# Optimization experiments

Measured on AMD Instinct MI355X. Metric: run time of the kernel, lower is better.

The kernel has to match this reference:

```python
import jax, jax.numpy as jnp
import numpy as np

NUM_M = 512
NUM_T = 64
MAX_STEPS = 20
TAU = 1.0


def setup_inputs() -> dict:
    key = jax.random.key(0)
    ks = jax.random.split(key, 10)
    num_m, num_t = NUM_M, NUM_T
    inp = {
        "v_src": jax.random.normal(ks[0], (1, num_m), jnp.float32),
        "v_target": jax.random.normal(ks[1], (1, num_m), jnp.float32),
        # small-magnitude generators so matrix_exp stays well-conditioned
        "omegas": jax.random.normal(ks[2], (num_t, num_m, num_m), jnp.float32) * 0.01,
        "W1": jax.random.normal(ks[3], (2 * num_m, 256), jnp.float32) * (1.0 / np.sqrt(2 * num_m)),
        "b1": jnp.zeros((256,), jnp.float32),
        "W2": jax.random.normal(ks[4], (256, 128), jnp.float32) * (1.0 / np.sqrt(256)),
        "b2": jnp.zeros((128,), jnp.float32),
        "W3": jax.random.normal(ks[5], (128, num_t), jnp.float32) * (1.0 / np.sqrt(128)),
        "b3": jnp.zeros((num_t,), jnp.float32),
        # pre-sampled gumbel noise, one draw per step: [max_steps, B, num_t]
        "gumbel_noise": jax.random.gumbel(ks[6], (MAX_STEPS, 1, num_t), jnp.float32),
    }
    return inp


def reference(v_src, v_target, omegas, W1, b1, W2, b2, W3, b3, gumbel_noise):
    tgt_idx = jnp.argmax(v_target, axis=-1)  # [B]

    def mlp(x):
        h = jax.nn.relu(x @ W1 + b1)
        h = jax.nn.relu(h @ W2 + b2)
        return h @ W3 + b3  # [B, num_t]

    batched_expm = jax.vmap(jax.scipy.linalg.expm)

    def step(carry, g):
        v, done = carry  # v: [B, num_m], done: [B] bool
        x = jnp.concatenate([v, v_target], axis=-1)        # [B, 2*num_m]
        logits = mlp(x)                                     # [B, num_t]
        # gumbel_softmax(tau=1.0, hard=False)
        soft = jax.nn.softmax((logits + g) / TAU, axis=-1)
        omega_k = jnp.einsum('bt,tmk->bmk', soft, omegas)   # [B, m, m]
        R_k = batched_expm(omega_k)                         # [B, m, m]
        v_new = jnp.einsum('bmk,bk->bm', R_k, v)            # [B, m]
        # freeze state and zero-pad logits once the target marking was reached
        v_out = jnp.where(done[:, None], v, v_new)
        logits_out = jnp.where(done[:, None], jnp.zeros_like(logits), logits)
        done_new = done | (jnp.argmax(v_new, axis=-1) == tgt_idx)
        return (v_out, done_new), logits_out

    done0 = jnp.zeros((v_src.shape[0],), bool)
    (v_final, _), logits_seq = jax.lax.scan(step, (v_src, done0), gumbel_noise)
    # logits_seq: [max_steps, B, num_t]; B==1 -> [max_steps, num_t] (torch squeeze(0))
    return v_final, logits_seq[:, 0, :]
```

## Files before the change

### kernel.cpp

```cpp
#include <hip/hip_runtime.h>
#include <hip/hip_fp16.h>


#define NBLK 256
#define NTHR 512
#define NSTEP 20
#define NTAY 3
#define RBUF 4

typedef unsigned long long ull;

#define XW(buf, i) (X + ((((buf) << 8) + (i)) << 3))

__device__ __forceinline__ float wredsum(float p) {
#pragma unroll
  for (int off = 32; off > 0; off >>= 1) p += __shfl_xor(p, off, 64);
  return p;
}

__device__ __forceinline__ void publish2(ull* w, float v0, float v1, unsigned int tag2) {
  unsigned int u0 = (__float_as_uint(v0) & ~3u) | tag2;
  ull x = (ull)u0 | ((ull)__float_as_uint(v1) << 32);
  __hip_atomic_store(w, x, __ATOMIC_RELAXED, __HIP_MEMORY_SCOPE_AGENT);
}

__device__ __forceinline__ float2 poll2(ull* w, unsigned int tag2) {
  int it = 0;
  for (;;) {
    ull x = __hip_atomic_load(w, __ATOMIC_RELAXED, __HIP_MEMORY_SCOPE_AGENT);
    if ((unsigned int)(x & 3u) == tag2) {
      float2 r;
      r.x = __uint_as_float((unsigned int)x);
      r.y = __uint_as_float((unsigned int)(x >> 32));
      return r;
    }
    if (it == 0)      __builtin_amdgcn_s_sleep(1);
    else if (it == 1) __builtin_amdgcn_s_sleep(2);
    else              __builtin_amdgcn_s_sleep(4);
    if (it < 2) ++it;
  }
}

__global__ __launch_bounds__(NTHR) void petri_kernel(
    const float* __restrict__ vsrc, const float* __restrict__ vtgt,
    const float* __restrict__ omg,  const float* __restrict__ W1,
    const float* __restrict__ b1,   const float* __restrict__ W2,
    const float* __restrict__ b2,   const float* __restrict__ W3,
    const float* __restrict__ b3,   const float* __restrict__ gum,
    ull* __restrict__ X, float* __restrict__ out) {
  __shared__ __half2 oh[64 * 512];
  __shared__ float A0_s[512], A1_s[512];
  __shared__ float v_loc[512], tgt_s[512], w_s[512];
  __shared__ float w1c_s[1024];
  __shared__ float gum_s[NSTEP * 64];
  __shared__ float b2_s[128], b3_s[64];
  __shared__ float soft_s[64], h1_s[256], h2_s[128];
  __shared__ float redp[512];
  __shared__ float rf8[8];
  __shared__ int   ri8[8];
  __shared__ float acc2[2];
  __shared__ int   bc[1];

  const int b = blockIdx.x, tid = threadIdx.x;
  const int wv = tid >> 6, ln = tid & 63;

  v_loc[tid] = vsrc[tid];
  tgt_s[tid] = vtgt[tid];
  w1c_s[tid] = W1[tid * 256 + b];
  w1c_s[tid + 512] = W1[(tid + 512) * 256 + b];
  for (int i = tid; i < NSTEP * 64; i += NTHR) gum_s[i] = gum[i];
  if (tid >= 512 - 128) {
    int j = tid - (512 - 128);
    b2_s[j] = b2[j];
    if (j < 64) b3_s[j] = b3[j];
  }
  float w2r[64];
  {
    const int o = tid & 127, q = tid >> 7;
    const float* p = W2 + ((q << 6) * 128) + o;
#pragma unroll
    for (int i = 0; i < 64; ++i) w2r[i] = p[i * 128];
  }
  float w3r[16];
  {
    const int o = tid & 63, q = tid >> 6;
    const float* p = W3 + ((q << 4) * 64) + o;
#pragma unroll
    for (int i = 0; i < 16; ++i) w3r[i] = p[i * 64];
  }
  {
    const float* base0 = omg + (b << 10) + tid;
#pragma unroll 4
    for (int t = 0; t < 64; ++t) {
      float x0 = base0[t * 262144];
      float x1 = base0[t * 262144 + 512];
      oh[t * 512 + tid] = __floats2half2_rn(x0, x1);
    }
  }
  __syncthreads();

  int tgtIdx;
  {
    float v = tgt_s[tid]; int ix = tid;
#pragma unroll
    for (int off = 32; off > 0; off >>= 1) {
      float ov = __shfl_xor(v, off, 64); int oi = __shfl_xor(ix, off, 64);
      if (ov > v || (ov == v && oi < ix)) { v = ov; ix = oi; }
    }
    if (ln == 0) { rf8[wv] = v; ri8[wv] = ix; }
    __syncthreads();
    if (tid == 0) {
      float bv = rf8[0]; int bix = ri8[0];
      for (int q = 1; q < 8; ++q)
        if (rf8[q] > bv || (rf8[q] == bv && ri8[q] < bix)) { bv = rf8[q]; bix = ri8[q]; }
      bc[0] = bix;
    }
    __syncthreads();
    tgtIdx = bc[0];
    __syncthreads();
  }

  int d = 0;
  int r = 0;

  for (int s = 0; s < NSTEP; ++s) {
    if (d) {
      if (b == 0 && tid < 64) out[512 + s * 64 + tid] = 0.0f;
      continue;
    }

    {
      const int buf = r & (RBUF - 1);
      const unsigned int tg = (unsigned int)((r >> 2) & 3);
      float p = fmaf(v_loc[tid], w1c_s[tid], tgt_s[tid] * w1c_s[tid + 512]);
      p = wredsum(p);
      if (ln == 0) rf8[wv] = p;
      __syncthreads();
      if (tid == 0) {
        float a = b1[b];
        for (int q = 0; q < 8; ++q) a += rf8[q];
        float h = fmaxf(a, 0.f);
        publish2(XW(buf, b), h, h, tg);
      }
      if (tid < 256) h1_s[tid] = poll2(XW(buf, tid), tg).x;
      __syncthreads();
      ++r;
    }

    {
      const int q = tid >> 7;
      float a = 0.f;
      const float* hp = h1_s + (q << 6);
#pragma unroll
      for (int i = 0; i < 64; ++i) a = fmaf(hp[i], w2r[i], a);
      redp[tid] = a;
    }
    __syncthreads();
    if (tid < 128) {
      float rr = redp[tid] + redp[tid + 128] + redp[tid + 256] + redp[tid + 384] + b2_s[tid];
      h2_s[tid] = fmaxf(rr, 0.f);
    }
    __syncthreads();
    {
      const int q = tid >> 6;
      float a = 0.f;
      const float* hp = h2_s + (q << 4);
#pragma unroll
      for (int i = 0; i < 16; ++i) a = fmaf(hp[i], w3r[i], a);
      redp[tid] = a;
    }
    __syncthreads();
    if (tid < 64) {
      float a = b3_s[tid];
#pragma unroll
      for (int q = 0; q < 8; ++q) a += redp[tid + (q << 6)];
      float lg = a + gum_s[s * 64 + tid];
      float mx = lg;
#pragma unroll
      for (int off = 32; off > 0; off >>= 1) mx = fmaxf(mx, __shfl_xor(mx, off, 64));
      float e = __expf(lg - mx);
      float sm = e;
#pragma unroll
      for (int off = 32; off > 0; off >>= 1) sm += __shfl_xor(sm, off, 64);
      soft_s[tid] = e / sm;
      if (b == 0) out[512 + s * 64 + tid] = a;
    }
    __syncthreads();

    {
      float a0 = 0.f, a1 = 0.f;
#pragma unroll 8
      for (int t = 0; t < 64; ++t) {
        float2 xy = __half22float2(oh[t * 512 + tid]);
        float sv = soft_s[t];
        a0 = fmaf(sv, xy.x, a0);
        a1 = fmaf(sv, xy.y, a1);
      }
      A0_s[tid] = a0; A1_s[tid] = a1;
    }
    __syncthreads();

    {
      const int buf = r & (RBUF - 1);
      const unsigned int tg = (unsigned int)((r >> 2) & 3);
      const float* Ar = (tid < 256) ? A0_s : A1_s;
      const int j = tid & 255;
      float p = fmaf(Ar[j], v_loc[j], Ar[j + 256] * v_loc[j + 256]);
      p = wredsum(p);
      if (ln == 0) rf8[wv] = p;
      __syncthreads();
      if (tid == 0) {
        float s0 = rf8[0] + rf8[1] + rf8[2] + rf8[3];
        float s1 = rf8[4] + rf8[5] + rf8[6] + rf8[7];
        acc2[0] = v_loc[(b << 1)] + s0;
        acc2[1] = v_loc[(b << 1) + 1] + s1;
        publish2(XW(buf, b), s0, s1, tg);
      }
      if (tid < 256) {
        float2 g = poll2(XW(buf, tid), tg);
        w_s[(tid << 1)] = g.x;
        w_s[(tid << 1) + 1] = g.y;
      }
      __syncthreads();
      ++r;
    }

    for (int n = 2; n <= NTAY; ++n) {
      const int buf = r & (RBUF - 1);
      const unsigned int tg = (unsigned int)((r >> 2) & 3);
      const float* Ar = (tid < 256) ? A0_s : A1_s;
      const int j = tid & 255;
      float p = fmaf(Ar[j], w_s[j], Ar[j + 256] * w_s[j + 256]);
      p = wredsum(p);
      if (ln == 0) rf8[wv] = p;
      __syncthreads();
      if (tid == 0) {
        const float inv = 1.0f / (float)n;
        float s0 = (rf8[0] + rf8[1] + rf8[2] + rf8[3]) * inv;
        float s1 = (rf8[4] + rf8[5] + rf8[6] + rf8[7]) * inv;
        acc2[0] += s0; acc2[1] += s1;
        float p0 = (n < NTAY) ? s0 : acc2[0];
        float p1 = (n < NTAY) ? s1 : acc2[1];
        publish2(XW(buf, b), p0, p1, tg);
      }
      if (n < NTAY) {
        if (tid < 256) {
          float2 g = poll2(XW(buf, tid), tg);
          w_s[(tid << 1)] = g.x;
          w_s[(tid << 1) + 1] = g.y;
        }
        __syncthreads();
        ++r;
      } else {
        if (tid < 256) {
          float2 g = poll2(XW(buf, tid), tg);
          v_loc[(tid << 1)] = g.x;
          v_loc[(tid << 1) + 1] = g.y;
        }
        __syncthreads();
        float v = v_loc[tid]; int ix = tid;
#pragma unroll
        for (int off = 32; off > 0; off >>= 1) {
          float ov = __shfl_xor(v, off, 64); int oi = __shfl_xor(ix, off, 64);
          if (ov > v || (ov == v && oi < ix)) { v = ov; ix = oi; }
        }
        if (ln == 0) { rf8[wv] = v; ri8[wv] = ix; }
        __syncthreads();
        if (tid == 0) {
          float bv = rf8[0]; int bix = ri8[0];
          for (int q = 1; q < 8; ++q)
            if (rf8[q] > bv || (rf8[q] == bv && ri8[q] < bix)) { bv = rf8[q]; bix = ri8[q]; }
          bc[0] = (bix == tgtIdx) ? 1 : 0;
        }
        __syncthreads();
        if (bc[0]) d = 1;
        __syncthreads();
        ++r;
      }
    }
  }

  if (b == 0) out[tid] = v_loc[tid];
}

extern "C" void kernel_launch(void* const* d_in, const int* in_sizes, int n_in,
                              void* d_out, int out_size, void* d_ws, size_t ws_size,
                              hipStream_t stream) {
  (void)in_sizes; (void)n_in; (void)out_size; (void)ws_size;
  petri_kernel<<<dim3(NBLK), dim3(NTHR), 0, stream>>>(
      (const float*)d_in[0], (const float*)d_in[1], (const float*)d_in[2],
      (const float*)d_in[3], (const float*)d_in[4], (const float*)d_in[5],
      (const float*)d_in[6], (const float*)d_in[7], (const float*)d_in[8],
      (const float*)d_in[9], (ull*)d_ws, (float*)d_out);
}
```

Measured before the change: 364.0 us.

## Replicate cross-block exchange slots to spread polling contention

Each block now publishes its value to up to 8 replicated slots, and each group of blocks polls its own replica, so fewer pollers hit the same cache lines. The backoff sleeps in the poll loop are removed so waiting blocks spin tightly. The ring shrinks from 4 to 2 buffers, which shortens the tag cycle, and the replica count is chosen to fit the workspace. The cost is more stores per publish and heavier memory traffic from tight spinning.

```diff
diff --git a/kernel.cpp b/kernel.cpp
--- a/kernel.cpp
+++ b/kernel.cpp
@@ -6,11 +6,9 @@
 #define NTHR 512
 #define NSTEP 20
 #define NTAY 3
-#define RBUF 4
+#define RBUF 2
 
 typedef unsigned long long ull;
-
-#define XW(buf, i) (X + ((((buf) << 8) + (i)) << 3))
 
 __device__ __forceinline__ float wredsum(float p) {
 #pragma unroll
@@ -18,14 +16,21 @@
   return p;
 }
 
-__device__ __forceinline__ void publish2(ull* w, float v0, float v1, unsigned int tag2) {
+__device__ __forceinline__ ull* xw(ull* X, int buf, int word, int rep, int k) {
+  return X + ((((buf << 8) + word) << k) + rep) * 8;
+}
+
+__device__ __forceinline__ void publishR(ull* X, int buf, int word, int k,
+                                         float v0, float v1, unsigned int tag2) {
   unsigned int u0 = (__float_as_uint(v0) & ~3u) | tag2;
   ull x = (ull)u0 | ((ull)__float_as_uint(v1) << 32);
-  __hip_atomic_store(w, x, __ATOMIC_RELAXED, __HIP_MEMORY_SCOPE_AGENT);
-}
-
-__device__ __forceinline__ float2 poll2(ull* w, unsigned int tag2) {
-  int it = 0;
+  const int nrep = 1 << k;
+  for (int rp = 0; rp < nrep; ++rp)
+    __hip_atomic_store(xw(X, buf, word, rp, k), x, __ATOMIC_RELAXED,
+                       __HIP_MEMORY_SCOPE_AGENT);
+}
+
+__device__ __forceinline__ float2 pollR(ull* w, unsigned int tag2) {
   for (;;) {
     ull x = __hip_atomic_load(w, __ATOMIC_RELAXED, __HIP_MEMORY_SCOPE_AGENT);
     if ((unsigned int)(x & 3u) == tag2) {
@@ -34,10 +39,6 @@
       r.y = __uint_as_float((unsigned int)(x >> 32));
       return r;
     }
-    if (it == 0)      __builtin_amdgcn_s_sleep(1);
-    else if (it == 1) __builtin_amdgcn_s_sleep(2);
-    else              __builtin_amdgcn_s_sleep(4);
-    if (it < 2) ++it;
   }
 }
 
@@ -47,7 +48,7 @@
     const float* __restrict__ b1,   const float* __restrict__ W2,
     const float* __restrict__ b2,   const float* __restrict__ W3,
     const float* __restrict__ b3,   const float* __restrict__ gum,
-    ull* __restrict__ X, float* __restrict__ out) {
+    ull* __restrict__ X, float* __restrict__ out, int repk) {
   __shared__ __half2 oh[64 * 512];
   __shared__ float A0_s[512], A1_s[512];
   __shared__ float v_loc[512], tgt_s[512], w_s[512];
@@ -63,6 +64,7 @@
 
   const int b = blockIdx.x, tid = threadIdx.x;
   const int wv = tid >> 6, ln = tid & 63;
+  const int myrep = (b << repk) >> 8;
 
   v_loc[tid] = vsrc[tid];
   tgt_s[tid] = vtgt[tid];
@@ -131,7 +133,7 @@
 
     {
       const int buf = r & (RBUF - 1);
-      const unsigned int tg = (unsigned int)((r >> 2) & 3);
+      const unsigned int tg = (unsigned int)((r >> 1) & 3);
       float p = fmaf(v_loc[tid], w1c_s[tid], tgt_s[tid] * w1c_s[tid + 512]);
       p = wredsum(p);
       if (ln == 0) rf8[wv] = p;
@@ -140,9 +142,9 @@
         float a = b1[b];
         for (int q = 0; q < 8; ++q) a += rf8[q];
         float h = fmaxf(a, 0.f);
-        publish2(XW(buf, b), h, h, tg);
-      }
-      if (tid < 256) h1_s[tid] = poll2(XW(buf, tid), tg).x;
+        publishR(X, buf, b, repk, h, h, tg);
+      }
+      if (tid < 256) h1_s[tid] = pollR(xw(X, buf, tid, myrep, repk), tg).x;
       __syncthreads();
       ++r;
     }
@@ -202,7 +204,7 @@
 
     {
       const int buf = r & (RBUF - 1);
-      const unsigned int tg = (unsigned int)((r >> 2) & 3);
+      const unsigned int tg = (unsigned int)((r >> 1) & 3);
       const float* Ar = (tid < 256) ? A0_s : A1_s;
       const int j = tid & 255;
       float p = fmaf(Ar[j], v_loc[j], Ar[j + 256] * v_loc[j + 256]);
@@ -214,10 +216,10 @@
         float s1 = rf8[4] + rf8[5] + rf8[6] + rf8[7];
         acc2[0] = v_loc[(b << 1)] + s0;
         acc2[1] = v_loc[(b << 1) + 1] + s1;
-        publish2(XW(buf, b), s0, s1, tg);
+        publishR(X, buf, b, repk, s0, s1, tg);
       }
       if (tid < 256) {
-        float2 g = poll2(XW(buf, tid), tg);
+        float2 g = pollR(xw(X, buf, tid, myrep, repk), tg);
         w_s[(tid << 1)] = g.x;
         w_s[(tid << 1) + 1] = g.y;
       }
@@ -227,7 +229,7 @@
 
     for (int n = 2; n <= NTAY; ++n) {
       const int buf = r & (RBUF - 1);
-      const unsigned int tg = (unsigned int)((r >> 2) & 3);
+      const unsigned int tg = (unsigned int)((r >> 1) & 3);
       const float* Ar = (tid < 256) ? A0_s : A1_s;
       const int j = tid & 255;
       float p = fmaf(Ar[j], w_s[j], Ar[j + 256] * w_s[j + 256]);
@@ -241,11 +243,11 @@
         acc2[0] += s0; acc2[1] += s1;
         float p0 = (n < NTAY) ? s0 : acc2[0];
         float p1 = (n < NTAY) ? s1 : acc2[1];
-        publish2(XW(buf, b), p0, p1, tg);
+        publishR(X, buf, b, repk, p0, p1, tg);
       }
       if (n < NTAY) {
         if (tid < 256) {
-          float2 g = poll2(XW(buf, tid), tg);
+          float2 g = pollR(xw(X, buf, tid, myrep, repk), tg);
           w_s[(tid << 1)] = g.x;
           w_s[(tid << 1) + 1] = g.y;
         }
@@ -253,7 +255,7 @@
         ++r;
       } else {
         if (tid < 256) {
-          float2 g = poll2(XW(buf, tid), tg);
+          float2 g = pollR(xw(X, buf, tid, myrep, repk), tg);
           v_loc[(tid << 1)] = g.x;
           v_loc[(tid << 1) + 1] = g.y;
         }
@@ -286,10 +288,13 @@
 extern "C" void kernel_launch(void* const* d_in, const int* in_sizes, int n_in,
                               void* d_out, int out_size, void* d_ws, size_t ws_size,
                               hipStream_t stream) {
-  (void)in_sizes; (void)n_in; (void)out_size; (void)ws_size;
+  (void)in_sizes; (void)n_in; (void)out_size;
+  int repk = 3;
+  while (repk > 0 && (size_t)(RBUF * 256 * 64) * (size_t)(1 << repk) > ws_size)
+    --repk;
   petri_kernel<<<dim3(NBLK), dim3(NTHR), 0, stream>>>(
       (const float*)d_in[0], (const float*)d_in[1], (const float*)d_in[2],
       (const float*)d_in[3], (const float*)d_in[4], (const float*)d_in[5],
       (const float*)d_in[6], (const float*)d_in[7], (const float*)d_in[8],
-      (const float*)d_in[9], (ull*)d_ws, (float*)d_out);
-}
+      (const float*)d_in[9], (ull*)d_ws, (float*)d_out, repk);
+}
```

Measured after the change: 430.7 us. 1.18x slower.
